# Optimization experiments

Hardware: AMD Instinct MI355X
Metric: run time of the kernel (lower is better)

The kernel has to match this reference:

```python
import jax, jax.numpy as jnp
import numpy as np

LN_EPS = 1e-5


def setup_inputs() -> dict:
    key = jax.random.key(0)
    ks = jax.random.split(key, 6)
    B, N, C, H = 8, 4096, 768, 12
    D = C // H
    x = jax.random.normal(ks[0], (B, N, C), dtype=jnp.float32)
    w_qkv = jax.random.normal(ks[1], (3 * C, C), dtype=jnp.float32) * (C ** -0.5)
    w_proj = jax.random.normal(ks[2], (C, C), dtype=jnp.float32) * (C ** -0.5)
    b_proj = jnp.zeros((C,), dtype=jnp.float32)
    # trunc_normal_(std=0.02) approximated by clipped normal
    p1 = jnp.clip(jax.random.normal(ks[3], (H, N), dtype=jnp.float32) * 0.02, -0.04, 0.04)
    p2 = jnp.clip(jax.random.normal(ks[4], (H, N), dtype=jnp.float32) * 0.02, -0.04, 0.04)
    gamma = jnp.ones((D,), dtype=jnp.float32)
    beta = jnp.zeros((D,), dtype=jnp.float32)
    return {"x": x, "w_qkv": w_qkv, "w_proj": w_proj, "b_proj": b_proj,
            "p1": p1, "p2": p2, "gamma": gamma, "beta": beta}


def _layernorm(h, gamma, beta):
    mu = jnp.mean(h, axis=-1, keepdims=True)
    var = jnp.var(h, axis=-1, keepdims=True)
    return (h - mu) * jax.lax.rsqrt(var + LN_EPS) * gamma + beta


def reference(x, w_qkv, w_proj, b_proj, p1, p2, gamma, beta):
    B, N, C = x.shape
    H = p1.shape[0]
    D = C // H
    # qkv projection (no bias): [B,N,3C] -> [3,B,H,N,D]
    qkv = (x @ w_qkv.T).reshape(B, N, 3, H, D).transpose(2, 0, 3, 1, 4)
    q, k, v = qkv[0], qkv[1], qkv[2]
    # weighted k*v reduction over sequence: [B,H,D]
    modulator = jnp.einsum('hn,bhnd->bhd', p2, k * v)
    modulator = _layernorm(modulator, gamma, beta)
    # broadcast modulation back over N: [B,H,N,D]
    modulator = jnp.einsum('hn,bhd->bhnd', p1, modulator)
    out = (q * modulator).transpose(0, 2, 1, 3).reshape(B, N, C)
    return out @ w_proj.T + b_proj
```

## Files before the change

kernel.cpp:

```cpp
#include <hip/hip_runtime.h>
#include <stdint.h>
#include <stddef.h>

#define LN_EPS 1e-5f

typedef __bf16 bf16;
typedef __bf16 bf16x8 __attribute__((ext_vector_type(8)));
typedef __bf16 bf16x4 __attribute__((ext_vector_type(4)));
typedef float f32x4 __attribute__((ext_vector_type(4)));

#define GL16(gp, lp)                                                                   \
  __builtin_amdgcn_global_load_lds((__attribute__((address_space(1))) uint32_t*)(gp),  \
                                   (__attribute__((address_space(3))) uint32_t*)(lp),  \
                                   16, 0, 0)

#define XV4   6291456
#define WQV4  442368
#define WPV4  147456
__global__ __launch_bounds__(256) void cvt_all(const float* __restrict__ x,
                                               const float* __restrict__ wq,
                                               const float* __restrict__ wp,
                                               bf16* __restrict__ xb,
                                               bf16* __restrict__ wqb,
                                               bf16* __restrict__ wpb) {
  int i = blockIdx.x * 256 + threadIdx.x;
  const float* src; bf16* dst; int off;
  if (i < XV4)              { src = x;  dst = xb;  off = i; }
  else if (i < XV4 + WQV4)  { src = wq; dst = wqb; off = i - XV4; }
  else                      { src = wp; dst = wpb; off = i - (XV4 + WQV4); }
  const float4 v = ((const float4*)src)[off];
  bf16x4 o;
  o[0] = (bf16)v.x; o[1] = (bf16)v.y; o[2] = (bf16)v.z; o[3] = (bf16)v.w;
  ((bf16x4*)dst)[off] = o;
}

__device__ __forceinline__ void gemm_core_768(const bf16* At, const bf16* Bt,
                                              bf16* lA, bf16* lB,
                                              f32x4 acc[4][4]) {
  const int tid  = threadIdx.x;
  const int wave = tid >> 6;
  const int lane = tid & 63;
  const int l16  = lane & 15;

  const int srow = wave * 32 + (lane >> 2);
  const int gq   = (lane & 3) ^ ((lane >> 3) & 3);
  const int scol = gq * 8;
  const bf16* gA0 = At + srow * 768 + scol;
  const bf16* gA1 = gA0 + 16 * 768;
  const bf16* gB0 = Bt + srow * 768 + scol;
  const bf16* gB1 = gB0 + 16 * 768;
  bf16* sA0 = lA + wave * 1024 + lane * 8;
  bf16* sA1 = sA0 + 512;
  bf16* sB0 = lB + wave * 1024 + lane * 8;
  bf16* sB1 = sB0 + 512;

  const int wm = (wave & 1) * 64;
  const int wn = (wave >> 1) * 64;
  const int qg = lane >> 4;
  const int sw = (l16 >> 1) & 3;
  const int rdoff = ((qg ^ sw) * 8);

  for (int kt = 0; kt < 768; kt += 32) {
    GL16(gA0 + kt, sA0);
    GL16(gA1 + kt, sA1);
    GL16(gB0 + kt, sB0);
    GL16(gB1 + kt, sB1);
    __syncthreads();

    bf16x8 aF[4], bF[4];
#pragma unroll
    for (int i = 0; i < 4; i++)
      aF[i] = *(const bf16x8*)(lA + (wm + i * 16 + l16) * 32 + rdoff);
#pragma unroll
    for (int j = 0; j < 4; j++)
      bF[j] = *(const bf16x8*)(lB + (wn + j * 16 + l16) * 32 + rdoff);

#pragma unroll
    for (int i = 0; i < 4; i++)
#pragma unroll
      for (int j = 0; j < 4; j++)
        acc[i][j] = __builtin_amdgcn_mfma_f32_16x16x32_bf16(aF[i], bF[j], acc[i][j], 0, 0, 0);

    __syncthreads();
  }
}

__global__ __launch_bounds__(256) void kv_gemm_reduce(const bf16* __restrict__ A,
                                                      const bf16* __restrict__ B,
                                                      const float* __restrict__ p2,
                                                      float* __restrict__ partials) {
  __shared__ __align__(16) bf16 sKV[2 * 128 * 68];
  __shared__ float red[4][64];
  bf16* lA = sKV;
  bf16* lB = sKV + 4096;

  const int h    = blockIdx.x;
  const int mblk = blockIdx.y;
  const int m0   = mblk * 128;
  const int tid  = threadIdx.x, wave = tid >> 6, lane = tid & 63;

  const bf16* Bt = B + (size_t)(wave < 2 ? (768 + h * 64) : (1536 + h * 64 - 64)) * 768;

  f32x4 acc[4][4] = {};
  gemm_core_768(A + (size_t)m0 * 768, Bt, lA, lB, acc);

  const int kv    = wave >> 1;
  const int row_l = (wave & 1) * 64 + (lane >> 4) * 4;
  const int d_l   = lane & 15;
  bf16* sT = sKV + kv * (128 * 68);
#pragma unroll
  for (int i = 0; i < 4; i++)
#pragma unroll
    for (int j = 0; j < 4; j++)
#pragma unroll
      for (int r = 0; r < 4; r++)
        sT[(row_l + i * 16 + r) * 68 + j * 16 + d_l] = (bf16)acc[i][j][r];
  __syncthreads();

  const int d  = tid & 63;
  const int ch = tid >> 6;
  const int n_base = (m0 & 4095) + ch * 32;
  const float* pw = p2 + h * 4096 + n_base;
  const bf16* sk = sKV + (ch * 32) * 68 + d;
  const bf16* sv = sk + 128 * 68;
  float s = 0.f;
#pragma unroll 8
  for (int n = 0; n < 32; n++)
    s += pw[n] * (float)sk[n * 68] * (float)sv[n * 68];
  red[ch][d] = s;
  __syncthreads();
  if (tid < 64) {
    partials[((size_t)mblk * 12 + h) * 64 + tid] =
        red[0][tid] + red[1][tid] + red[2][tid] + red[3][tid];
  }
}

__global__ __launch_bounds__(64) void mod_reduce_ln(const float* __restrict__ partials,
                                                    const float* __restrict__ gamma,
                                                    const float* __restrict__ beta,
                                                    float* __restrict__ mod) {
  const int h = blockIdx.x, b = blockIdx.y;
  const int d = threadIdx.x;

  const float* p = partials + ((size_t)(b * 32) * 12 + h) * 64 + d;
  float s = 0.f;
#pragma unroll 8
  for (int mb = 0; mb < 32; mb++) s += p[(size_t)mb * 12 * 64];

  float sum = s, sumsq = s * s;
#pragma unroll
  for (int o = 32; o > 0; o >>= 1) {
    sum   += __shfl_xor(sum, o);
    sumsq += __shfl_xor(sumsq, o);
  }
  const float mu  = sum * (1.f / 64.f);
  const float var = sumsq * (1.f / 64.f) - mu * mu;
  const float r   = rsqrtf(var + LN_EPS);
  mod[(b * 12 + h) * 64 + d] = (s - mu) * r * gamma[d] + beta[d];
}

__global__ __launch_bounds__(256) void q_gemm_mod(const bf16* __restrict__ A,
                                                  const bf16* __restrict__ B,
                                                  const float* __restrict__ p1,
                                                  const float* __restrict__ mod,
                                                  bf16* __restrict__ amod) {
  __shared__ __align__(16) bf16 lA[128 * 32];
  __shared__ __align__(16) bf16 lB[128 * 32];
  f32x4 acc[4][4] = {};

  const int n0 = blockIdx.x * 128;
  const int m0 = blockIdx.y * 128;
  gemm_core_768(A + (size_t)m0 * 768, B + (size_t)n0 * 768, lA, lB, acc);

  const int tid = threadIdx.x, wave = tid >> 6, lane = tid & 63;
  const int row0 = m0 + (wave & 1) * 64 + (lane >> 4) * 4;
  const int col0 = n0 + (wave >> 1) * 64 + (lane & 15);
  const int b    = m0 >> 12;
  const int h    = (n0 + (wave >> 1) * 64) >> 6;

  float p1v[4][4];
#pragma unroll
  for (int i = 0; i < 4; i++)
#pragma unroll
    for (int r = 0; r < 4; r++)
      p1v[i][r] = p1[h * 4096 + ((row0 + i * 16 + r) & 4095)];
  float mv[4];
#pragma unroll
  for (int j = 0; j < 4; j++) mv[j] = mod[b * 768 + col0 + j * 16];

#pragma unroll
  for (int i = 0; i < 4; i++)
#pragma unroll
    for (int j = 0; j < 4; j++)
#pragma unroll
      for (int r = 0; r < 4; r++)
        amod[(size_t)(row0 + i * 16 + r) * 768 + col0 + j * 16] =
            (bf16)(acc[i][j][r] * p1v[i][r] * mv[j]);
}

__global__ __launch_bounds__(256) void gemm_proj(const bf16* __restrict__ A,
                                                 const bf16* __restrict__ B,
                                                 const float* __restrict__ bias,
                                                 float* __restrict__ C) {
  __shared__ __align__(16) bf16 lA[128 * 32];
  __shared__ __align__(16) bf16 lB[128 * 32];
  f32x4 acc[4][4] = {};

  const int n0 = blockIdx.x * 128;
  const int m0 = blockIdx.y * 128;
  gemm_core_768(A + (size_t)m0 * 768, B + (size_t)n0 * 768, lA, lB, acc);

  const int tid = threadIdx.x, wave = tid >> 6, lane = tid & 63;
  const int row0 = m0 + (wave & 1) * 64 + (lane >> 4) * 4;
  const int col0 = n0 + (wave >> 1) * 64 + (lane & 15);
#pragma unroll
  for (int j = 0; j < 4; j++) {
    const int col = col0 + j * 16;
    const float bv = bias[col];
#pragma unroll
    for (int i = 0; i < 4; i++)
#pragma unroll
      for (int r = 0; r < 4; r++)
        C[(size_t)(row0 + i * 16 + r) * 768 + col] = acc[i][j][r] + bv;
  }
}

extern "C" void kernel_launch(void* const* d_in, const int* in_sizes, int n_in,
                              void* d_out, int out_size, void* d_ws, size_t ws_size,
                              hipStream_t stream) {
  (void)in_sizes; (void)n_in; (void)out_size; (void)ws_size;

  const float* x      = (const float*)d_in[0];
  const float* w_qkv  = (const float*)d_in[1];
  const float* w_proj = (const float*)d_in[2];
  const float* b_proj = (const float*)d_in[3];
  const float* p1     = (const float*)d_in[4];
  const float* p2     = (const float*)d_in[5];
  const float* gamma  = (const float*)d_in[6];
  const float* beta   = (const float*)d_in[7];
  float* out = (float*)d_out;

  char* ws = (char*)d_ws;
  bf16*  xb       = (bf16*)(ws + 0);
  bf16*  wqb      = (bf16*)(ws + 50331648);
  bf16*  wpb      = (bf16*)(ws + 53870592);
  bf16*  amod     = (bf16*)(ws + 55050240);
  float* partials = (float*)(ws + 105381888);
  float* mod      = (float*)(ws + 106168320);

  cvt_all<<<26880, 256, 0, stream>>>(x, w_qkv, w_proj, xb, wqb, wpb);

  kv_gemm_reduce<<<dim3(12, 256), 256, 0, stream>>>(xb, wqb, p2, partials);

  mod_reduce_ln<<<dim3(12, 8), 64, 0, stream>>>(partials, gamma, beta, mod);

  q_gemm_mod<<<dim3(6, 256), 256, 0, stream>>>(xb, wqb, p1, mod, amod);

  gemm_proj<<<dim3(6, 256), 256, 0, stream>>>(amod, wpb, b_proj, out);
}
```

Baseline: 407.5 us.

## Replace GEMM core with 256x256 multi-stage pipelined LDS kernel and block swizzle

Replaces the single-buffered 128x128 GEMM core with a 512-thread 256x256 tile kernel. It uses a four-slot LDS ring fed by global_load_lds, explicit vmcnt waits and barriers, and s_setprio around the MFMA bursts, so loads overlap compute. All three GEMM kernels adopt it, with a block-index remap for L2 locality. The kv reduction now handles two heads per block, so the partials reduction count changes to match. The larger tiles raise data reuse but hold 128 KB of LDS and many accumulator registers per block, which may limit occupancy.

```diff
diff --git a/kernel.cpp b/kernel.cpp
--- a/kernel.cpp
+++ b/kernel.cpp
@@ -13,6 +13,11 @@
   __builtin_amdgcn_global_load_lds((__attribute__((address_space(1))) uint32_t*)(gp),  \
                                    (__attribute__((address_space(3))) uint32_t*)(lp),  \
                                    16, 0, 0)
+
+#define SBAR   asm volatile("s_barrier" ::: "memory")
+#define LGK0   asm volatile("s_waitcnt lgkmcnt(0)" ::: "memory")
+#define VMW(N) asm volatile("s_waitcnt vmcnt(" #N ")" ::: "memory")
+#define NOWAIT ((void)0)
 
 #define XV4   6291456
 #define WQV4  442368
@@ -34,104 +39,139 @@
   ((bf16x4*)dst)[off] = o;
 }
 
-__device__ __forceinline__ void gemm_core_768(const bf16* At, const bf16* Bt,
-                                              bf16* lA, bf16* lB,
-                                              f32x4 acc[4][4]) {
+#define STAGE_A(T, KH, SLOT) do {                      \
+    GL16(pA0 + (T)*64 + (KH)*32, dA + (SLOT)*8192);    \
+    GL16(pA1 + (T)*64 + (KH)*32, dA + (SLOT)*8192 + 4096); } while (0)
+
+#define STAGE_B(T, KH, SLOT) do {                      \
+    GL16(pB0 + (T)*64 + (KH)*32, dB + (SLOT)*8192);    \
+    GL16(pB1 + (T)*64 + (KH)*32, dB + (SLOT)*8192 + 4096); } while (0)
+
+#define PHASE(SLOT, MH, RB, STG, WAIT) do {                                         \
+    if (RB) {                                                                       \
+      _Pragma("unroll") for (int n = 0; n < 4; ++n)                                 \
+        bF[n] = *(const bf16x8*)(ldsB + (SLOT)*8192 + (rB + n*16)*32 + colE);       \
+    }                                                                               \
+    _Pragma("unroll") for (int m = 0; m < 4; ++m)                                   \
+      aF[m] = *(const bf16x8*)(ldsA + (SLOT)*8192 + (rA + (MH)*64 + m*16)*32 + colE); \
+    STG;                                                                            \
+    SBAR;                                                                           \
+    LGK0;                                                                           \
+    __builtin_amdgcn_sched_barrier(0);                                              \
+    __builtin_amdgcn_s_setprio(1);                                                  \
+    _Pragma("unroll") for (int m = 0; m < 4; ++m)                                   \
+      _Pragma("unroll") for (int n = 0; n < 4; ++n)                                 \
+        acc[(MH)*4 + m][n] =                                                        \
+            __builtin_amdgcn_mfma_f32_16x16x32_bf16(aF[m], bF[n],                   \
+                                                    acc[(MH)*4 + m][n], 0, 0, 0);   \
+    __builtin_amdgcn_s_setprio(0);                                                  \
+    WAIT;                                                                           \
+    SBAR;                                                                           \
+  } while (0)
+
+#define TILE(SB, ST1, ST2, ST3, ST4, W2, W4) do { \
+    PHASE((SB),     0, true,  ST1, NOWAIT);       \
+    PHASE((SB),     1, false, ST2, W2);           \
+    PHASE((SB) + 1, 0, true,  ST3, NOWAIT);       \
+    PHASE((SB) + 1, 1, false, ST4, W4);           \
+  } while (0)
+
+__device__ __forceinline__ void gemm256(const bf16* pA0, const bf16* pA1,
+                                        const bf16* pB0, const bf16* pB1,
+                                        bf16* sh, f32x4 acc[8][4]) {
   const int tid  = threadIdx.x;
+  const int lane = tid & 63;
   const int wave = tid >> 6;
-  const int lane = tid & 63;
+  const int wm   = wave >> 2;
+  const int wn   = wave & 3;
   const int l16  = lane & 15;
-
-  const int srow = wave * 32 + (lane >> 2);
-  const int gq   = (lane & 3) ^ ((lane >> 3) & 3);
-  const int scol = gq * 8;
-  const bf16* gA0 = At + srow * 768 + scol;
-  const bf16* gA1 = gA0 + 16 * 768;
-  const bf16* gB0 = Bt + srow * 768 + scol;
-  const bf16* gB1 = gB0 + 16 * 768;
-  bf16* sA0 = lA + wave * 1024 + lane * 8;
-  bf16* sA1 = sA0 + 512;
-  bf16* sB0 = lB + wave * 1024 + lane * 8;
-  bf16* sB1 = sB0 + 512;
-
-  const int wm = (wave & 1) * 64;
-  const int wn = (wave >> 1) * 64;
-  const int qg = lane >> 4;
-  const int sw = (l16 >> 1) & 3;
-  const int rdoff = ((qg ^ sw) * 8);
-
-  for (int kt = 0; kt < 768; kt += 32) {
-    GL16(gA0 + kt, sA0);
-    GL16(gA1 + kt, sA1);
-    GL16(gB0 + kt, sB0);
-    GL16(gB1 + kt, sB1);
-    __syncthreads();
-
-    bf16x8 aF[4], bF[4];
-#pragma unroll
-    for (int i = 0; i < 4; i++)
-      aF[i] = *(const bf16x8*)(lA + (wm + i * 16 + l16) * 32 + rdoff);
-#pragma unroll
-    for (int j = 0; j < 4; j++)
-      bF[j] = *(const bf16x8*)(lB + (wn + j * 16 + l16) * 32 + rdoff);
-
-#pragma unroll
-    for (int i = 0; i < 4; i++)
-#pragma unroll
-      for (int j = 0; j < 4; j++)
-        acc[i][j] = __builtin_amdgcn_mfma_f32_16x16x32_bf16(aF[i], bF[j], acc[i][j], 0, 0, 0);
-
-    __syncthreads();
-  }
-}
-
-__global__ __launch_bounds__(256) void kv_gemm_reduce(const bf16* __restrict__ A,
-                                                      const bf16* __restrict__ B,
-                                                      const float* __restrict__ p2,
-                                                      float* __restrict__ partials) {
-  __shared__ __align__(16) bf16 sKV[2 * 128 * 68];
-  __shared__ float red[4][64];
-  bf16* lA = sKV;
-  bf16* lB = sKV + 4096;
-
-  const int h    = blockIdx.x;
-  const int mblk = blockIdx.y;
-  const int m0   = mblk * 128;
-  const int tid  = threadIdx.x, wave = tid >> 6, lane = tid & 63;
-
-  const bf16* Bt = B + (size_t)(wave < 2 ? (768 + h * 64) : (1536 + h * 64 - 64)) * 768;
-
-  f32x4 acc[4][4] = {};
-  gemm_core_768(A + (size_t)m0 * 768, Bt, lA, lB, acc);
-
-  const int kv    = wave >> 1;
-  const int row_l = (wave & 1) * 64 + (lane >> 4) * 4;
-  const int d_l   = lane & 15;
-  bf16* sT = sKV + kv * (128 * 68);
-#pragma unroll
-  for (int i = 0; i < 4; i++)
-#pragma unroll
-    for (int j = 0; j < 4; j++)
-#pragma unroll
-      for (int r = 0; r < 4; r++)
-        sT[(row_l + i * 16 + r) * 68 + j * 16 + d_l] = (bf16)acc[i][j][r];
+  const int colE = ((((lane >> 4) * 16) ^ (((l16 >> 1) & 3) << 4)) >> 1);
+  bf16* const ldsA = sh;
+  bf16* const ldsB = sh + 32768;
+  bf16* const dA   = ldsA + tid * 8;
+  bf16* const dB   = ldsB + tid * 8;
+  const int rA = wm * 128 + l16;
+  const int rB = wn * 64 + l16;
+  bf16x8 aF[4], bF[4];
+
+  STAGE_A(0, 0, 0); STAGE_B(0, 0, 0);
+  STAGE_A(0, 1, 1); STAGE_B(0, 1, 1);
+  STAGE_A(1, 0, 2); STAGE_B(1, 0, 2);
+  VMW(8);
+  SBAR;
+
+  for (int T = 0; T < 10; T += 2) {
+    TILE(0, STAGE_A(T+1,1,3), STAGE_B(T+1,1,3), STAGE_A(T+2,0,0), STAGE_B(T+2,0,0), VMW(8), VMW(8));
+    TILE(2, STAGE_A(T+2,1,1), STAGE_B(T+2,1,1), STAGE_A(T+3,0,2), STAGE_B(T+3,0,2), VMW(8), VMW(8));
+  }
+  TILE(0, STAGE_A(11,1,3), STAGE_B(11,1,3), NOWAIT, NOWAIT, VMW(8), VMW(4));
+  TILE(2, NOWAIT, NOWAIT, NOWAIT, NOWAIT, VMW(0), NOWAIT);
+
+  asm volatile("s_waitcnt vmcnt(0) lgkmcnt(0)" ::: "memory");
   __syncthreads();
-
-  const int d  = tid & 63;
-  const int ch = tid >> 6;
-  const int n_base = (m0 & 4095) + ch * 32;
-  const float* pw = p2 + h * 4096 + n_base;
-  const bf16* sk = sKV + (ch * 32) * 68 + d;
-  const bf16* sv = sk + 128 * 68;
+}
+
+__global__ __launch_bounds__(512, 2) void kv_gemm_reduce(const bf16* __restrict__ A,
+                                                         const bf16* __restrict__ B,
+                                                         const float* __restrict__ p2,
+                                                         float* __restrict__ partials) {
+  __shared__ __align__(16) bf16 sh[65536];
+  __shared__ float red[4][2][64];
+
+  int lin = blockIdx.y * 6 + blockIdx.x;
+  lin = (lin & 7) * 96 + (lin >> 3);
+  const int hh   = lin % 6;
+  const int mblk = lin / 6;
+  const int m0   = mblk * 256;
+  const int h0   = hh * 2;
+
+  const int tid = threadIdx.x;
+  const int rr  = tid >> 2;
+  const int ck  = ((tid & 3) ^ ((tid >> 3) & 3)) * 8;
+  const bf16* pA0 = A + (size_t)(m0 + rr) * 768 + ck;
+  const bf16* pA1 = pA0 + (size_t)128 * 768;
+  const int r1 = 128 + rr;
+  const int wr0 = 768 + (((rr >> 6) & 1) * 768) + (h0 + (rr >> 7)) * 64 + (rr & 63);
+  const int wr1 = 768 + (((r1 >> 6) & 1) * 768) + (h0 + (r1 >> 7)) * 64 + (r1 & 63);
+  const bf16* pB0 = B + (size_t)wr0 * 768 + ck;
+  const bf16* pB1 = B + (size_t)wr1 * 768 + ck;
+
+  f32x4 acc[8][4] = {};
+  gemm256(pA0, pA1, pB0, pB1, sh, acc);
+
+  const int lane = tid & 63, wave = tid >> 6;
+  const int wm = wave >> 2, wn = wave & 3, l16 = lane & 15;
+  const int crow0 = wm * 128 + (lane >> 4) * 4;
+  const int ccol0 = wn * 64 + l16;
+#pragma unroll
+  for (int mi = 0; mi < 8; ++mi)
+#pragma unroll
+    for (int ni = 0; ni < 4; ++ni)
+#pragma unroll
+      for (int r = 0; r < 4; ++r) {
+        const int row = crow0 + mi * 16 + r;
+        const int col = ccol0 + ni * 16;
+        sh[row * 256 + (col ^ (((row >> 2) & 3) << 4))] = (bf16)acc[mi][ni][r];
+      }
+  __syncthreads();
+
+  const int chunk = tid >> 7, hl = (tid >> 6) & 1, d = tid & 63;
+  const float* pw = p2 + (size_t)(h0 + hl) * 4096 + (m0 & 4095) + chunk * 64;
   float s = 0.f;
 #pragma unroll 8
-  for (int n = 0; n < 32; n++)
-    s += pw[n] * (float)sk[n * 68] * (float)sv[n * 68];
-  red[ch][d] = s;
+  for (int n = 0; n < 64; ++n) {
+    const int row = chunk * 64 + n;
+    const int x = ((row >> 2) & 3) << 4;
+    const float kk = (float)sh[row * 256 + ((hl * 128 + d) ^ x)];
+    const float vv = (float)sh[row * 256 + ((hl * 128 + 64 + d) ^ x)];
+    s += pw[n] * kk * vv;
+  }
+  red[chunk][hl][d] = s;
   __syncthreads();
-  if (tid < 64) {
-    partials[((size_t)mblk * 12 + h) * 64 + tid] =
-        red[0][tid] + red[1][tid] + red[2][tid] + red[3][tid];
+  if (tid < 128) {
+    const int hx = tid >> 6, dd = tid & 63;
+    partials[((size_t)mblk * 12 + h0 + hx) * 64 + dd] =
+        red[0][hx][dd] + red[1][hx][dd] + red[2][hx][dd] + red[3][hx][dd];
   }
 }
 
@@ -142,10 +182,10 @@
   const int h = blockIdx.x, b = blockIdx.y;
   const int d = threadIdx.x;
 
-  const float* p = partials + ((size_t)(b * 32) * 12 + h) * 64 + d;
+  const float* p = partials + ((size_t)(b * 16) * 12 + h) * 64 + d;
   float s = 0.f;
-#pragma unroll 8
-  for (int mb = 0; mb < 32; mb++) s += p[(size_t)mb * 12 * 64];
+#pragma unroll
+  for (int mb = 0; mb < 16; ++mb) s += p[(size_t)mb * 12 * 64];
 
   float sum = s, sumsq = s * s;
 #pragma unroll
@@ -159,69 +199,91 @@
   mod[(b * 12 + h) * 64 + d] = (s - mu) * r * gamma[d] + beta[d];
 }
 
-__global__ __launch_bounds__(256) void q_gemm_mod(const bf16* __restrict__ A,
-                                                  const bf16* __restrict__ B,
-                                                  const float* __restrict__ p1,
-                                                  const float* __restrict__ mod,
-                                                  bf16* __restrict__ amod) {
-  __shared__ __align__(16) bf16 lA[128 * 32];
-  __shared__ __align__(16) bf16 lB[128 * 32];
-  f32x4 acc[4][4] = {};
-
-  const int n0 = blockIdx.x * 128;
-  const int m0 = blockIdx.y * 128;
-  gemm_core_768(A + (size_t)m0 * 768, B + (size_t)n0 * 768, lA, lB, acc);
-
-  const int tid = threadIdx.x, wave = tid >> 6, lane = tid & 63;
-  const int row0 = m0 + (wave & 1) * 64 + (lane >> 4) * 4;
-  const int col0 = n0 + (wave >> 1) * 64 + (lane & 15);
+__global__ __launch_bounds__(512, 2) void q_gemm_mod(const bf16* __restrict__ A,
+                                                     const bf16* __restrict__ B,
+                                                     const float* __restrict__ p1,
+                                                     const float* __restrict__ mod,
+                                                     bf16* __restrict__ amod) {
+  __shared__ __align__(16) bf16 sh[65536];
+
+  int lin = blockIdx.y * 3 + blockIdx.x;
+  lin = (lin & 7) * 48 + (lin >> 3);
+  const int n0 = (lin % 3) * 256;
+  const int m0 = (lin / 3) * 256;
+
+  const int tid = threadIdx.x;
+  const int rr  = tid >> 2;
+  const int ck  = ((tid & 3) ^ ((tid >> 3) & 3)) * 8;
+  const bf16* pA0 = A + (size_t)(m0 + rr) * 768 + ck;
+  const bf16* pA1 = pA0 + (size_t)128 * 768;
+  const bf16* pB0 = B + (size_t)(n0 + rr) * 768 + ck;
+  const bf16* pB1 = pB0 + (size_t)128 * 768;
+
+  f32x4 acc[8][4] = {};
+  gemm256(pA0, pA1, pB0, pB1, sh, acc);
+
+  const int lane = tid & 63, wave = tid >> 6;
+  const int wm = wave >> 2, wn = wave & 3, l16 = lane & 15;
+  const int row0 = m0 + wm * 128 + (lane >> 4) * 4;
+  const int col0 = n0 + wn * 64 + l16;
   const int b    = m0 >> 12;
-  const int h    = (n0 + (wave >> 1) * 64) >> 6;
-
-  float p1v[4][4];
-#pragma unroll
-  for (int i = 0; i < 4; i++)
-#pragma unroll
-    for (int r = 0; r < 4; r++)
-      p1v[i][r] = p1[h * 4096 + ((row0 + i * 16 + r) & 4095)];
+  const int h    = (n0 >> 6) + wn;
+
+  float p1v[8][4];
+#pragma unroll
+  for (int mi = 0; mi < 8; ++mi)
+#pragma unroll
+    for (int r = 0; r < 4; ++r)
+      p1v[mi][r] = p1[(size_t)h * 4096 + ((row0 + mi * 16 + r) & 4095)];
   float mv[4];
 #pragma unroll
-  for (int j = 0; j < 4; j++) mv[j] = mod[b * 768 + col0 + j * 16];
-
-#pragma unroll
-  for (int i = 0; i < 4; i++)
-#pragma unroll
-    for (int j = 0; j < 4; j++)
-#pragma unroll
-      for (int r = 0; r < 4; r++)
-        amod[(size_t)(row0 + i * 16 + r) * 768 + col0 + j * 16] =
-            (bf16)(acc[i][j][r] * p1v[i][r] * mv[j]);
-}
-
-__global__ __launch_bounds__(256) void gemm_proj(const bf16* __restrict__ A,
-                                                 const bf16* __restrict__ B,
-                                                 const float* __restrict__ bias,
-                                                 float* __restrict__ C) {
-  __shared__ __align__(16) bf16 lA[128 * 32];
-  __shared__ __align__(16) bf16 lB[128 * 32];
-  f32x4 acc[4][4] = {};
-
-  const int n0 = blockIdx.x * 128;
-  const int m0 = blockIdx.y * 128;
-  gemm_core_768(A + (size_t)m0 * 768, B + (size_t)n0 * 768, lA, lB, acc);
-
-  const int tid = threadIdx.x, wave = tid >> 6, lane = tid & 63;
-  const int row0 = m0 + (wave & 1) * 64 + (lane >> 4) * 4;
-  const int col0 = n0 + (wave >> 1) * 64 + (lane & 15);
-#pragma unroll
-  for (int j = 0; j < 4; j++) {
-    const int col = col0 + j * 16;
+  for (int ni = 0; ni < 4; ++ni) mv[ni] = mod[b * 768 + col0 + ni * 16];
+
+#pragma unroll
+  for (int mi = 0; mi < 8; ++mi)
+#pragma unroll
+    for (int ni = 0; ni < 4; ++ni)
+#pragma unroll
+      for (int r = 0; r < 4; ++r)
+        amod[(size_t)(row0 + mi * 16 + r) * 768 + col0 + ni * 16] =
+            (bf16)(acc[mi][ni][r] * p1v[mi][r] * mv[ni]);
+}
+
+__global__ __launch_bounds__(512, 2) void gemm_proj(const bf16* __restrict__ A,
+                                                    const bf16* __restrict__ B,
+                                                    const float* __restrict__ bias,
+                                                    float* __restrict__ C) {
+  __shared__ __align__(16) bf16 sh[65536];
+
+  int lin = blockIdx.y * 3 + blockIdx.x;
+  lin = (lin & 7) * 48 + (lin >> 3);
+  const int n0 = (lin % 3) * 256;
+  const int m0 = (lin / 3) * 256;
+
+  const int tid = threadIdx.x;
+  const int rr  = tid >> 2;
+  const int ck  = ((tid & 3) ^ ((tid >> 3) & 3)) * 8;
+  const bf16* pA0 = A + (size_t)(m0 + rr) * 768 + ck;
+  const bf16* pA1 = pA0 + (size_t)128 * 768;
+  const bf16* pB0 = B + (size_t)(n0 + rr) * 768 + ck;
+  const bf16* pB1 = pB0 + (size_t)128 * 768;
+
+  f32x4 acc[8][4] = {};
+  gemm256(pA0, pA1, pB0, pB1, sh, acc);
+
+  const int lane = tid & 63, wave = tid >> 6;
+  const int wm = wave >> 2, wn = wave & 3, l16 = lane & 15;
+  const int row0 = m0 + wm * 128 + (lane >> 4) * 4;
+  const int col0 = n0 + wn * 64 + l16;
+#pragma unroll
+  for (int ni = 0; ni < 4; ++ni) {
+    const int col = col0 + ni * 16;
     const float bv = bias[col];
 #pragma unroll
-    for (int i = 0; i < 4; i++)
-#pragma unroll
-      for (int r = 0; r < 4; r++)
-        C[(size_t)(row0 + i * 16 + r) * 768 + col] = acc[i][j][r] + bv;
+    for (int mi = 0; mi < 8; ++mi)
+#pragma unroll
+      for (int r = 0; r < 4; ++r)
+        C[(size_t)(row0 + mi * 16 + r) * 768 + col] = acc[mi][ni][r] + bv;
   }
 }
 
@@ -250,11 +312,11 @@
 
   cvt_all<<<26880, 256, 0, stream>>>(x, w_qkv, w_proj, xb, wqb, wpb);
 
-  kv_gemm_reduce<<<dim3(12, 256), 256, 0, stream>>>(xb, wqb, p2, partials);
+  kv_gemm_reduce<<<dim3(6, 128), 512, 0, stream>>>(xb, wqb, p2, partials);
 
   mod_reduce_ln<<<dim3(12, 8), 64, 0, stream>>>(partials, gamma, beta, mod);
 
-  q_gemm_mod<<<dim3(6, 256), 256, 0, stream>>>(xb, wqb, p1, mod, amod);
-
-  gemm_proj<<<dim3(6, 256), 256, 0, stream>>>(amod, wpb, b_proj, out);
-}
+  q_gemm_mod<<<dim3(3, 128), 512, 0, stream>>>(xb, wqb, p1, mod, amod);
+
+  gemm_proj<<<dim3(3, 128), 512, 0, stream>>>(amod, wpb, b_proj, out);
+}
```

Measured after the change: 379.5 us. 1.07x faster.
